# Kernel tuning notes

Measured on AMD Instinct MI355X. Metric: run time of the kernel, lower is better.

## Reference

```python
import jax, jax.numpy as jnp
import numpy as np

DIM, H, HD = 512, 8, 64
N_BANK = 4096
EPS = 1e-5


def layernorm(x, g, b):
    m = jnp.mean(x, axis=-1, keepdims=True)
    v = jnp.mean(jnp.square(x - m), axis=-1, keepdims=True)
    return (x - m) * jax.lax.rsqrt(v + EPS) * g + b


def setup_inputs() -> dict:
    key = jax.random.key(0)
    ks = jax.random.split(key, 8)
    # xavier_uniform bound for square (512,512) linears
    bound = float(np.sqrt(6.0 / (DIM + DIM)))
    inp = {
        "x_q": jax.random.normal(ks[0], (32, 128, DIM), jnp.float32),
        "x_k": jax.random.normal(ks[1], (N_BANK, DIM), jnp.float32),
        "x_v": jax.random.normal(ks[2], (N_BANK, DIM), jnp.float32),
        "Wq": jax.random.uniform(ks[3], (DIM, DIM), jnp.float32, -bound, bound),
        "Wk": jax.random.uniform(ks[4], (DIM, DIM), jnp.float32, -bound, bound),
        "Wv": jax.random.uniform(ks[5], (DIM, DIM), jnp.float32, -bound, bound),
        "Wproj": jax.random.uniform(ks[6], (DIM, DIM), jnp.float32, -bound, bound),
        "qn_g": jnp.ones((HD,), jnp.float32),
        "qn_b": jnp.zeros((HD,), jnp.float32),
        "kn_g": jnp.ones((HD,), jnp.float32),
        "kn_b": jnp.zeros((HD,), jnp.float32),
        "n_g": jnp.ones((DIM,), jnp.float32),
        "n_b": jnp.zeros((DIM,), jnp.float32),
    }
    return inp


def reference(x_q, x_k, x_v, Wq, Wk, Wv, Wproj, qn_g, qn_b, kn_g, kn_b, n_g, n_b):
    B, S, D = x_q.shape
    N = x_k.shape[0]
    scale = HD ** (-0.5)
    # Linear layers (torch: y = x @ W.T)
    q = jnp.einsum('bsd,od->bso', x_q, Wq).reshape(B, S, H, HD).transpose(0, 2, 1, 3)  # (B,H,S,hd)
    k = jnp.einsum('nd,od->no', x_k, Wk).reshape(N, H, HD).transpose(1, 0, 2)          # (H,N,hd)
    v = jnp.einsum('nd,od->no', x_v, Wv).reshape(N, H, HD).transpose(1, 0, 2)          # (H,N,hd)
    # per-head qk layernorm
    q = layernorm(q, qn_g, qn_b) * scale
    k = layernorm(k, kn_g, kn_b)
    # cross-attention to shared bank (K/V have no batch dim)
    attn = jnp.einsum('bhsd,hnd->bhsn', q, k)          # (B,H,S,N)
    attn = jax.nn.softmax(attn, axis=-1)
    x = jnp.einsum('bhsn,hnd->bhsd', attn, v)          # (B,H,S,hd)
    x = x.transpose(0, 2, 1, 3).reshape(B, S, D)
    x = layernorm(x, n_g, n_b)
    x = jnp.einsum('bsd,od->bso', x, Wproj)
    return x
```

## Files before the change

kernel.cpp:

```cpp
#include <hip/hip_runtime.h>
#include <hip/hip_bf16.h>
#include <math.h>

#define DIM 512
#define NHEAD 8
#define HD 64
#define NBANK 4096
#define NQROWS 4096
#define EPS 1e-5f
#define QSCALE 0.125f
#define PART_ELEMS (NQROWS * DIM)

typedef __attribute__((ext_vector_type(4))) float floatx4;
typedef __attribute__((ext_vector_type(8))) short short8;

__device__ __forceinline__ unsigned short f2bf(float f) {
    unsigned int u = __float_as_uint(f);
    u += 0x7fffu + ((u >> 16) & 1u);
    return (unsigned short)(u >> 16);
}
__device__ __forceinline__ float bf2f(unsigned short h) {
    return __uint_as_float(((unsigned int)h) << 16);
}
__device__ __forceinline__ unsigned int pk2(float a, float b) {
    union { __hip_bfloat162 h; unsigned int u; } cvt;
    cvt.h = __float22bfloat162_rn(make_float2(a, b));
    return cvt.u;
}
__device__ __forceinline__ void dma16(const void* gsrc, void* ldst) {
    __builtin_amdgcn_global_load_lds(
        (const __attribute__((address_space(1))) unsigned int*)gsrc,
        (__attribute__((address_space(3))) unsigned int*)ldst, 16, 0, 0);
}

__global__ __launch_bounds__(256) void wcvt_kernel(
    const float* __restrict__ Wq, const float* __restrict__ Wk,
    const float* __restrict__ Wv, const float* __restrict__ Wp,
    unsigned short* __restrict__ Wb)
{
    const float* src = (blockIdx.y == 0) ? Wq : (blockIdx.y == 1) ? Wk
                     : (blockIdx.y == 2) ? Wv : Wp;
    unsigned short* dst = Wb + (size_t)blockIdx.y * DIM * DIM;
    const int i = (blockIdx.x * 256 + threadIdx.x) * 8;
    const int row = i >> 9, kpos = i & 511;
    const int kt = kpos >> 6, seg = (kpos >> 3) & 7;
    const float4 a0 = *(const float4*)(src + i);
    const float4 a1 = *(const float4*)(src + i + 4);
    union { short8 v; unsigned int u[4]; } t;
    t.u[0] = pk2(a0.x, a0.y); t.u[1] = pk2(a0.z, a0.w);
    t.u[2] = pk2(a1.x, a1.y); t.u[3] = pk2(a1.z, a1.w);
    *(short8*)(dst + (size_t)row * 512 + kt * 64 + ((seg ^ (row & 7)) << 3)) = t.v;
}

__global__ __launch_bounds__(256) void qkv_kernel(
    const float* __restrict__ xq, const float* __restrict__ xk, const float* __restrict__ xv,
    const unsigned short* __restrict__ Wb,
    const float* __restrict__ qg, const float* __restrict__ qbeta,
    const float* __restrict__ kg, const float* __restrict__ kbeta,
    unsigned short* __restrict__ Qb, unsigned short* __restrict__ Kb,
    unsigned short* __restrict__ VTb)
{
    __shared__ short8 smem[3072];
    const int tid  = threadIdx.x;
    const int w    = tid >> 6, lane = tid & 63, m = lane & 15, q = lane >> 4;
    const int wr   = w & 1, wc = w >> 1;
    const int row0 = blockIdx.x * 64;
    const int mat  = blockIdx.y >> 2;
    const int col0 = (blockIdx.y & 3) * 128;
    const float* X = (mat == 0) ? xq : (mat == 1) ? xk : xv;
    const unsigned short* Wm = Wb + (size_t)mat * DIM * DIM;

    const int arow0 = tid >> 3,           aseg = tid & 7;
    const int arow1 = (tid + 256) >> 3;
    const float* ap0 = X + (size_t)(row0 + arow0) * DIM + aseg * 8;
    const float* ap1 = X + (size_t)(row0 + arow1) * DIM + aseg * 8;
    const int adst0 = arow0 * 8 + (aseg ^ (arow0 & 7));
    const int adst1 = arow1 * 8 + (aseg ^ (arow1 & 7));
    const unsigned short* bsrc[4];
    #pragma unroll
    for (int j = 0; j < 4; ++j) {
        const int item = j * 256 + tid;
        bsrc[j] = Wm + (size_t)(col0 + (item >> 3)) * DIM + (item & 7) * 8;
    }

    floatx4 acc[2][4];
    #pragma unroll
    for (int mt = 0; mt < 2; ++mt)
        #pragma unroll
        for (int nt = 0; nt < 4; ++nt) acc[mt][nt] = (floatx4){0.f, 0.f, 0.f, 0.f};

    float4 pa[4];
    pa[0] = *(const float4*)(ap0);     pa[1] = *(const float4*)(ap0 + 4);
    pa[2] = *(const float4*)(ap1);     pa[3] = *(const float4*)(ap1 + 4);
    {
        short8* as = smem; short8* bs = smem + 512;
        union { short8 v; unsigned int u[4]; } ta;
        ta.u[0] = pk2(pa[0].x, pa[0].y); ta.u[1] = pk2(pa[0].z, pa[0].w);
        ta.u[2] = pk2(pa[1].x, pa[1].y); ta.u[3] = pk2(pa[1].z, pa[1].w);
        as[adst0] = ta.v;
        ta.u[0] = pk2(pa[2].x, pa[2].y); ta.u[1] = pk2(pa[2].z, pa[2].w);
        ta.u[2] = pk2(pa[3].x, pa[3].y); ta.u[3] = pk2(pa[3].z, pa[3].w);
        as[adst1] = ta.v;
        #pragma unroll
        for (int j = 0; j < 4; ++j)
            dma16(bsrc[j], bs + j * 256 + w * 64);
    }
    pa[0] = *(const float4*)(ap0 + 64);  pa[1] = *(const float4*)(ap0 + 68);
    pa[2] = *(const float4*)(ap1 + 64);  pa[3] = *(const float4*)(ap1 + 68);
    __syncthreads();

    for (int kt = 0; kt < 8; ++kt) {
        short8* as  = smem + (kt & 1) * 1536;
        short8* bs  = as + 512;
        short8* asn = smem + ((kt + 1) & 1) * 1536;
        short8* bsn = asn + 512;
        if (kt < 7) {
            union { short8 v; unsigned int u[4]; } ta;
            ta.u[0] = pk2(pa[0].x, pa[0].y); ta.u[1] = pk2(pa[0].z, pa[0].w);
            ta.u[2] = pk2(pa[1].x, pa[1].y); ta.u[3] = pk2(pa[1].z, pa[1].w);
            asn[adst0] = ta.v;
            ta.u[0] = pk2(pa[2].x, pa[2].y); ta.u[1] = pk2(pa[2].z, pa[2].w);
            ta.u[2] = pk2(pa[3].x, pa[3].y); ta.u[3] = pk2(pa[3].z, pa[3].w);
            asn[adst1] = ta.v;
            #pragma unroll
            for (int j = 0; j < 4; ++j)
                dma16(bsrc[j] + (kt + 1) * 64, bsn + j * 256 + w * 64);
        }
        if (kt < 6) {
            const int o = (kt + 2) * 64;
            pa[0] = *(const float4*)(ap0 + o);  pa[1] = *(const float4*)(ap0 + o + 4);
            pa[2] = *(const float4*)(ap1 + o);  pa[3] = *(const float4*)(ap1 + o + 4);
        }
        #pragma unroll
        for (int s = 0; s < 2; ++s) {
            short8 af[2], bfr[4];
            #pragma unroll
            for (int mt = 0; mt < 2; ++mt)
                af[mt] = as[(wr * 32 + mt * 16 + m) * 8 + ((s * 4 + q) ^ (m & 7))];
            #pragma unroll
            for (int nt = 0; nt < 4; ++nt)
                bfr[nt] = bs[(wc * 64 + nt * 16 + m) * 8 + ((s * 4 + q) ^ (m & 7))];
            #pragma unroll
            for (int mt = 0; mt < 2; ++mt)
                #pragma unroll
                for (int nt = 0; nt < 4; ++nt)
                    acc[mt][nt] = __builtin_amdgcn_mfma_f32_16x16x32_bf16(af[mt], bfr[nt], acc[mt][nt], 0, 0, 0);
        }
        __syncthreads();
    }

    if (mat < 2) {
        const float* g = (mat == 0) ? qg : kg;
        const float* be = (mat == 0) ? qbeta : kbeta;
        unsigned short* Y = (mat == 0) ? Qb : Kb;
        float gv[4], bv[4];
        #pragma unroll
        for (int nt = 0; nt < 4; ++nt) { gv[nt] = g[nt * 16 + m]; bv[nt] = be[nt * 16 + m]; }
        #pragma unroll
        for (int mt = 0; mt < 2; ++mt) {
            #pragma unroll
            for (int r = 0; r < 4; ++r) {
                float s = 0.f, sq = 0.f;
                #pragma unroll
                for (int nt = 0; nt < 4; ++nt) { const float v = acc[mt][nt][r]; s += v; sq += v * v; }
                s  += __shfl_xor(s, 1);  s  += __shfl_xor(s, 2);  s  += __shfl_xor(s, 4);  s  += __shfl_xor(s, 8);
                sq += __shfl_xor(sq, 1); sq += __shfl_xor(sq, 2); sq += __shfl_xor(sq, 4); sq += __shfl_xor(sq, 8);
                const float mean = s * (1.f / HD);
                const float var  = sq * (1.f / HD) - mean * mean;
                const float rr   = rsqrtf(var + EPS);
                const int grow = row0 + wr * 32 + mt * 16 + q * 4 + r;
                #pragma unroll
                for (int nt = 0; nt < 4; ++nt) {
                    float v = (acc[mt][nt][r] - mean) * rr * gv[nt] + bv[nt];
                    if (mat == 0) v *= QSCALE;
                    const int col = col0 + wc * 64 + nt * 16 + m;
                    int scol = col;
                    if (mat == 1) {
                        const int o = col & 63, sg2 = o >> 3;
                        scol = (col & ~63) | (((sg2 ^ (grow & 7)) << 3) | (o & 7));
                    }
                    Y[(size_t)grow * DIM + scol] = f2bf(v);
                }
            }
        }
    } else {
        unsigned short* vt = (unsigned short*)smem;
        __syncthreads();
        #pragma unroll
        for (int mt = 0; mt < 2; ++mt)
            #pragma unroll
            for (int nt = 0; nt < 4; ++nt) {
                const int c  = wc * 64 + nt * 16 + m;
                const int rw = wr * 32 + mt * 16 + q * 4;
                *(unsigned int*)(vt + c * 88 + rw)     = pk2(acc[mt][nt][0], acc[mt][nt][1]);
                *(unsigned int*)(vt + c * 88 + rw + 2) = pk2(acc[mt][nt][2], acc[mt][nt][3]);
            }
        __syncthreads();
        #pragma unroll
        for (int p = 0; p < 4; ++p) {
            const int idx = p * 256 + tid;
            const int c = idx >> 3, g = idx & 7;
            const int dglob = col0 + c, hh = dglob >> 6, dl = dglob & 63;
            const int pos = (g >> 2) * 32 + (g & 3) * 4;
            union { short8 v; ushort4 h4[2]; } tv;
            tv.h4[0] = *(const ushort4*)(vt + c * 88 + pos);
            tv.h4[1] = *(const ushort4*)(vt + c * 88 + pos + 16);
            *(short8*)(VTb + ((size_t)(hh * 64 + blockIdx.x) * 512
                              + dl * 8 + (g ^ (dl & 7))) * 8) = tv.v;
        }
    }
}

__global__ __launch_bounds__(256) void attn_kernel(
    const unsigned short* __restrict__ Qb, const unsigned short* __restrict__ Kb,
    const unsigned short* __restrict__ VTb, unsigned short* __restrict__ AOp,
    float* __restrict__ sums)
{
    __shared__ short8 smem[2048];
    const int tid  = threadIdx.x;
    const int w    = tid >> 6;
    const int lane = tid & 63;
    const int m    = lane & 15;
    const int Qd   = lane >> 4;
    const int h    = blockIdx.x & 7;
    const int qgi  = blockIdx.x >> 3;
    const int row0 = qgi * 128;
    const int part = blockIdx.y;
    const int c0   = part * 16;

    const int it0 = tid, it1 = tid + 256;
    const unsigned short* ksrc0 = Kb + (size_t)(it0 >> 3) * DIM + h * HD + (it0 & 7) * 8;
    const unsigned short* ksrc1 = Kb + (size_t)(it1 >> 3) * DIM + h * HD + (it1 & 7) * 8;
    const unsigned short* vbase = VTb + (size_t)h * 64 * 512 * 8;

    short8 qf[2][2];
    #pragma unroll
    for (int mt = 0; mt < 2; ++mt)
        #pragma unroll
        for (int s = 0; s < 2; ++s)
            qf[mt][s] = *(const short8*)(Qb + (size_t)(row0 + w * 32 + mt * 16 + m) * DIM
                                         + h * HD + s * 32 + Qd * 8);

    floatx4 of[4][2];
    float sump[2] = {0.f, 0.f};
    #pragma unroll
    for (int t = 0; t < 4; ++t)
        #pragma unroll
        for (int mt = 0; mt < 2; ++mt) of[t][mt] = (floatx4){0.f, 0.f, 0.f, 0.f};

    {
        short8* ks = smem; short8* vts = smem + 512;
        dma16(ksrc0 + (size_t)c0 * 64 * DIM, ks + w * 64);
        dma16(ksrc1 + (size_t)c0 * 64 * DIM, ks + 256 + w * 64);
        dma16(vbase + ((size_t)c0 * 512 + it0) * 8, vts + w * 64);
        dma16(vbase + ((size_t)c0 * 512 + it1) * 8, vts + 256 + w * 64);
    }
    __syncthreads();

    for (int c = 0; c < 16; ++c) {
        short8* ks  = smem + (c & 1) * 1024;
        short8* vts = ks + 512;
        if (c < 15) {
            short8* ksn  = smem + ((c + 1) & 1) * 1024;
            short8* vtsn = ksn + 512;
            const size_t nc = c0 + c + 1;
            dma16(ksrc0 + nc * 64 * DIM, ksn + w * 64);
            dma16(ksrc1 + nc * 64 * DIM, ksn + 256 + w * 64);
            dma16(vbase + (nc * 512 + it0) * 8, vtsn + w * 64);
            dma16(vbase + (nc * 512 + it1) * 8, vtsn + 256 + w * 64);
        }

        floatx4 st[4][2];
        #pragma unroll
        for (int t = 0; t < 4; ++t)
            #pragma unroll
            for (int mt = 0; mt < 2; ++mt) st[t][mt] = (floatx4){0.f, 0.f, 0.f, 0.f};
        #pragma unroll
        for (int s = 0; s < 2; ++s)
            #pragma unroll
            for (int t = 0; t < 4; ++t) {
                const short8 kf = ks[(t * 16 + m) * 8 + ((s * 4 + Qd) ^ (m & 7))];
                #pragma unroll
                for (int mt = 0; mt < 2; ++mt)
                    st[t][mt] = __builtin_amdgcn_mfma_f32_16x16x32_bf16(kf, qf[mt][s], st[t][mt], 0, 0, 0);
            }

        float p[4][2][4];
        #pragma unroll
        for (int t = 0; t < 4; ++t)
            #pragma unroll
            for (int mt = 0; mt < 2; ++mt)
                #pragma unroll
                for (int r = 0; r < 4; ++r) {
                    const float e = __expf(st[t][mt][r]);
                    p[t][mt][r] = e;
                    sump[mt] += e;
                }
        union { short8 v; unsigned int u[4]; } pf[2][2];
        #pragma unroll
        for (int mt = 0; mt < 2; ++mt)
            #pragma unroll
            for (int s2 = 0; s2 < 2; ++s2)
                #pragma unroll
                for (int u = 0; u < 4; ++u)
                    pf[mt][s2].u[u] = pk2(p[s2 * 2 + (u >> 1)][mt][(u & 1) * 2],
                                          p[s2 * 2 + (u >> 1)][mt][(u & 1) * 2 + 1]);

        #pragma unroll
        for (int s2 = 0; s2 < 2; ++s2)
            #pragma unroll
            for (int t2 = 0; t2 < 4; ++t2) {
                const short8 vf = vts[(t2 * 16 + m) * 8 + ((s2 * 4 + Qd) ^ (m & 7))];
                #pragma unroll
                for (int mt = 0; mt < 2; ++mt)
                    of[t2][mt] = __builtin_amdgcn_mfma_f32_16x16x32_bf16(vf, pf[mt][s2].v, of[t2][mt], 0, 0, 0);
            }
        __syncthreads();
    }

    #pragma unroll
    for (int mt = 0; mt < 2; ++mt) {
        float s = sump[mt];
        s += __shfl_xor(s, 16);
        s += __shfl_xor(s, 32);
        sump[mt] = s;
    }
    if (Qd == 0) {
        #pragma unroll
        for (int mt = 0; mt < 2; ++mt)
            sums[((size_t)part * NQROWS + row0 + w * 32 + mt * 16 + m) * NHEAD + h] = sump[mt];
    }

    unsigned int* ob = (unsigned int*)smem;
    #pragma unroll
    for (int t2 = 0; t2 < 4; ++t2)
        #pragma unroll
        for (int mt = 0; mt < 2; ++mt) {
            const int qq  = w * 32 + mt * 16 + m;
            const int blk = t2 * 2 + (Qd >> 1);
            const int sub = (Qd & 1) * 2;
            const int bs  = (blk ^ (qq & 7)) * 4;
            ob[qq * 32 + bs + sub]     = pk2(of[t2][mt][0], of[t2][mt][1]);
            ob[qq * 32 + bs + sub + 1] = pk2(of[t2][mt][2], of[t2][mt][3]);
        }
    __syncthreads();
    #pragma unroll
    for (int pp = 0; pp < 4; ++pp) {
        const int idx = tid + pp * 256;
        const int qq = idx >> 3, sg = idx & 7;
        *(short8*)(AOp + (size_t)part * PART_ELEMS + (size_t)(row0 + qq) * DIM + h * HD + sg * 8) =
            smem[qq * 8 + (sg ^ (qq & 7))];
    }
}

__global__ __launch_bounds__(256) void combine_kernel(
    const unsigned short* __restrict__ AOp, const float* __restrict__ sums,
    const float* __restrict__ g, const float* __restrict__ be,
    unsigned short* __restrict__ AO)
{
    __shared__ float rs[256], rq[256], sm[2], sr[2];
    const int tid  = threadIdx.x;
    const int half = tid >> 7;
    const int row  = blockIdx.x * 2 + half;
    const int t    = tid & 127;
    const int h    = t >> 4;

    float stot = 0.f;
    #pragma unroll
    for (int p = 0; p < 4; ++p)
        stot += sums[((size_t)p * NQROWS + row) * NHEAD + h];

    float o[4] = {0.f, 0.f, 0.f, 0.f};
    #pragma unroll
    for (int p = 0; p < 4; ++p) {
        const ushort4 u = *(const ushort4*)(AOp + (size_t)p * PART_ELEMS + (size_t)row * DIM + t * 4);
        o[0] += bf2f(u.x); o[1] += bf2f(u.y); o[2] += bf2f(u.z); o[3] += bf2f(u.w);
    }
    const float inv = 1.0f / stot;
    const float v0 = o[0] * inv, v1 = o[1] * inv, v2 = o[2] * inv, v3 = o[3] * inv;

    rs[tid] = v0 + v1 + v2 + v3;
    rq[tid] = v0 * v0 + v1 * v1 + v2 * v2 + v3 * v3;
    __syncthreads();
    #pragma unroll
    for (int off = 64; off > 0; off >>= 1) {
        if (t < off) { rs[tid] += rs[tid + off]; rq[tid] += rq[tid + off]; }
        __syncthreads();
    }
    if (t == 0) {
        const float mean = rs[tid] * (1.f / DIM);
        const float var  = rq[tid] * (1.f / DIM) - mean * mean;
        sm[half] = mean;
        sr[half] = rsqrtf(var + EPS);
    }
    __syncthreads();

    const float mean = sm[half], rstd = sr[half];
    const float4 g4 = *(const float4*)(g + t * 4);
    const float4 b4 = *(const float4*)(be + t * 4);
    uint2 packed;
    packed.x = pk2((v0 - mean) * rstd * g4.x + b4.x, (v1 - mean) * rstd * g4.y + b4.y);
    packed.y = pk2((v2 - mean) * rstd * g4.z + b4.z, (v3 - mean) * rstd * g4.w + b4.w);
    const int kt = t >> 4, seg = (t >> 1) & 7, jof = (t & 1) * 4;
    *(uint2*)(AO + (size_t)row * DIM + kt * 64 + ((seg ^ (row & 7)) << 3) + jof) = packed;
}

__global__ __launch_bounds__(256) void final_kernel(
    const unsigned short* __restrict__ AO, const unsigned short* __restrict__ Wpb,
    float* __restrict__ out)
{
    __shared__ short8 fs[2048];
    const int tid  = threadIdx.x;
    const int w    = tid >> 6, lane = tid & 63, m = lane & 15, q = lane >> 4;
    const int row0 = blockIdx.x * 64;
    const int col0 = blockIdx.y * 64;

    const int it0 = tid, it1 = tid + 256;
    const unsigned short* asrc0 = AO  + (size_t)(row0 + (it0 >> 3)) * DIM + (it0 & 7) * 8;
    const unsigned short* asrc1 = AO  + (size_t)(row0 + (it1 >> 3)) * DIM + (it1 & 7) * 8;
    const unsigned short* wsrc0 = Wpb + (size_t)(col0 + (it0 >> 3)) * DIM + (it0 & 7) * 8;
    const unsigned short* wsrc1 = Wpb + (size_t)(col0 + (it1 >> 3)) * DIM + (it1 & 7) * 8;

    floatx4 acc[4];
    #pragma unroll
    for (int mt = 0; mt < 4; ++mt) acc[mt] = (floatx4){0.f, 0.f, 0.f, 0.f};

    {
        dma16(asrc0, fs + w * 64);
        dma16(asrc1, fs + 256 + w * 64);
        dma16(wsrc0, fs + 512 + w * 64);
        dma16(wsrc1, fs + 768 + w * 64);
    }
    __syncthreads();

    for (int kt = 0; kt < 8; ++kt) {
        short8* buf  = fs + (kt & 1) * 1024;
        if (kt < 7) {
            short8* bufn = fs + ((kt + 1) & 1) * 1024;
            const int o = (kt + 1) * 64;
            dma16(asrc0 + o, bufn + w * 64);
            dma16(asrc1 + o, bufn + 256 + w * 64);
            dma16(wsrc0 + o, bufn + 512 + w * 64);
            dma16(wsrc1 + o, bufn + 768 + w * 64);
        }
        #pragma unroll
        for (int s = 0; s < 2; ++s) {
            short8 af[4];
            #pragma unroll
            for (int mt = 0; mt < 4; ++mt)
                af[mt] = buf[(mt * 16 + m) * 8 + ((s * 4 + q) ^ (m & 7))];
            const short8 bfr = buf[512 + (w * 16 + m) * 8 + ((s * 4 + q) ^ (m & 7))];
            #pragma unroll
            for (int mt = 0; mt < 4; ++mt)
                acc[mt] = __builtin_amdgcn_mfma_f32_16x16x32_bf16(af[mt], bfr, acc[mt], 0, 0, 0);
        }
        __syncthreads();
    }

    #pragma unroll
    for (int mt = 0; mt < 4; ++mt)
        #pragma unroll
        for (int r = 0; r < 4; ++r)
            out[(size_t)(row0 + mt * 16 + q * 4 + r) * DIM + col0 + w * 16 + m] = acc[mt][r];
}

extern "C" void kernel_launch(void* const* d_in, const int* in_sizes, int n_in,
                              void* d_out, int out_size, void* d_ws, size_t ws_size,
                              hipStream_t stream)
{
    const float* x_q = (const float*)d_in[0];
    const float* x_k = (const float*)d_in[1];
    const float* x_v = (const float*)d_in[2];
    const float* Wq  = (const float*)d_in[3];
    const float* Wk  = (const float*)d_in[4];
    const float* Wv  = (const float*)d_in[5];
    const float* Wp  = (const float*)d_in[6];
    const float* qg  = (const float*)d_in[7];
    const float* qb  = (const float*)d_in[8];
    const float* kg  = (const float*)d_in[9];
    const float* kb  = (const float*)d_in[10];
    const float* ng  = (const float*)d_in[11];
    const float* nb  = (const float*)d_in[12];
    float* out = (float*)d_out;

    unsigned short* Qb   = (unsigned short*)d_ws;
    unsigned short* Kb   = Qb  + (size_t)NQROWS * DIM;
    unsigned short* VTb  = Kb  + (size_t)NBANK * DIM;
    unsigned short* AOp  = VTb + (size_t)NBANK * DIM;
    float*          sums = (float*)(AOp + (size_t)4 * PART_ELEMS);
    unsigned short* Wb   = (unsigned short*)(sums + (size_t)4 * NQROWS * NHEAD);
    unsigned short* AO   = Qb;

    wcvt_kernel<<<dim3(128, 4), 256, 0, stream>>>(Wq, Wk, Wv, Wp, Wb);
    qkv_kernel<<<dim3(64, 12), 256, 0, stream>>>(x_q, x_k, x_v, Wb,
                                                 qg, qb, kg, kb, Qb, Kb, VTb);
    attn_kernel<<<dim3(256, 4), 256, 0, stream>>>(Qb, Kb, VTb, AOp, sums);
    combine_kernel<<<NQROWS / 2, 256, 0, stream>>>(AOp, sums, ng, nb, AO);
    final_kernel<<<dim3(64, 8), 256, 0, stream>>>(AO, Wb + (size_t)3 * DIM * DIM, out);
}
```

Baseline: 169.3 us.

## Pre-convert activations to bf16, DMA A tiles, use exp2 and MFMA row sums

The weight-conversion kernel now also converts x_q, x_k and x_v to swizzled bf16 in a workspace. This lets the QKV GEMM load its A tiles with direct global-to-LDS DMA instead of converting fp32 through registers. In attention, the softmax exponent uses exp2 with log2(e) folded into the Q scale, and row sums are computed with an extra MFMA against a ones vector instead of scalar adds and shuffles. The cost is an extra pass over the inputs plus a bf16 write and re-read, and sums are now taken from bf16-rounded probabilities.

```diff
diff --git a/kernel.cpp b/kernel.cpp
--- a/kernel.cpp
+++ b/kernel.cpp
@@ -8,11 +8,20 @@
 #define NBANK 4096
 #define NQROWS 4096
 #define EPS 1e-5f
-#define QSCALE 0.125f
+#define QSCALE 0.18033688011f
 #define PART_ELEMS (NQROWS * DIM)
 
 typedef __attribute__((ext_vector_type(4))) float floatx4;
 typedef __attribute__((ext_vector_type(8))) short short8;
+
+#if defined(__has_builtin)
+#if __has_builtin(__builtin_amdgcn_exp2f)
+#define EXP2(x) __builtin_amdgcn_exp2f(x)
+#endif
+#endif
+#ifndef EXP2
+#define EXP2(x) __expf((x) * 0.69314718056f)
+#endif
 
 __device__ __forceinline__ unsigned short f2bf(float f) {
     unsigned int u = __float_as_uint(f);
@@ -33,14 +42,24 @@
         (__attribute__((address_space(3))) unsigned int*)ldst, 16, 0, 0);
 }
 
-__global__ __launch_bounds__(256) void wcvt_kernel(
+__global__ __launch_bounds__(256) void cvt_kernel(
     const float* __restrict__ Wq, const float* __restrict__ Wk,
     const float* __restrict__ Wv, const float* __restrict__ Wp,
-    unsigned short* __restrict__ Wb)
-{
-    const float* src = (blockIdx.y == 0) ? Wq : (blockIdx.y == 1) ? Wk
-                     : (blockIdx.y == 2) ? Wv : Wp;
-    unsigned short* dst = Wb + (size_t)blockIdx.y * DIM * DIM;
+    const float* __restrict__ xq, const float* __restrict__ xk,
+    const float* __restrict__ xv,
+    unsigned short* __restrict__ Wb, unsigned short* __restrict__ Xb)
+{
+    const int y = blockIdx.y;
+    const float* src;
+    unsigned short* dst;
+    if (y < 4) {
+        if (blockIdx.x >= 128) return;
+        src = (y == 0) ? Wq : (y == 1) ? Wk : (y == 2) ? Wv : Wp;
+        dst = Wb + (size_t)y * DIM * DIM;
+    } else {
+        src = (y == 4) ? xq : (y == 5) ? xk : xv;
+        dst = Xb + (size_t)(y - 4) * NQROWS * DIM;
+    }
     const int i = (blockIdx.x * 256 + threadIdx.x) * 8;
     const int row = i >> 9, kpos = i & 511;
     const int kt = kpos >> 6, seg = (kpos >> 3) & 7;
@@ -53,8 +72,7 @@
 }
 
 __global__ __launch_bounds__(256) void qkv_kernel(
-    const float* __restrict__ xq, const float* __restrict__ xk, const float* __restrict__ xv,
-    const unsigned short* __restrict__ Wb,
+    const unsigned short* __restrict__ Xb, const unsigned short* __restrict__ Wb,
     const float* __restrict__ qg, const float* __restrict__ qbeta,
     const float* __restrict__ kg, const float* __restrict__ kbeta,
     unsigned short* __restrict__ Qb, unsigned short* __restrict__ Kb,
@@ -67,15 +85,12 @@
     const int row0 = blockIdx.x * 64;
     const int mat  = blockIdx.y >> 2;
     const int col0 = (blockIdx.y & 3) * 128;
-    const float* X = (mat == 0) ? xq : (mat == 1) ? xk : xv;
+    const unsigned short* Xm = Xb + (size_t)mat * NQROWS * DIM;
     const unsigned short* Wm = Wb + (size_t)mat * DIM * DIM;
 
-    const int arow0 = tid >> 3,           aseg = tid & 7;
-    const int arow1 = (tid + 256) >> 3;
-    const float* ap0 = X + (size_t)(row0 + arow0) * DIM + aseg * 8;
-    const float* ap1 = X + (size_t)(row0 + arow1) * DIM + aseg * 8;
-    const int adst0 = arow0 * 8 + (aseg ^ (arow0 & 7));
-    const int adst1 = arow1 * 8 + (aseg ^ (arow1 & 7));
+    const int it0 = tid, it1 = tid + 256;
+    const unsigned short* asrc0 = Xm + (size_t)(row0 + (it0 >> 3)) * DIM + (it0 & 7) * 8;
+    const unsigned short* asrc1 = Xm + (size_t)(row0 + (it1 >> 3)) * DIM + (it1 & 7) * 8;
     const unsigned short* bsrc[4];
     #pragma unroll
     for (int j = 0; j < 4; ++j) {
@@ -89,47 +104,28 @@
         #pragma unroll
         for (int nt = 0; nt < 4; ++nt) acc[mt][nt] = (floatx4){0.f, 0.f, 0.f, 0.f};
 
-    float4 pa[4];
-    pa[0] = *(const float4*)(ap0);     pa[1] = *(const float4*)(ap0 + 4);
-    pa[2] = *(const float4*)(ap1);     pa[3] = *(const float4*)(ap1 + 4);
     {
         short8* as = smem; short8* bs = smem + 512;
-        union { short8 v; unsigned int u[4]; } ta;
-        ta.u[0] = pk2(pa[0].x, pa[0].y); ta.u[1] = pk2(pa[0].z, pa[0].w);
-        ta.u[2] = pk2(pa[1].x, pa[1].y); ta.u[3] = pk2(pa[1].z, pa[1].w);
-        as[adst0] = ta.v;
-        ta.u[0] = pk2(pa[2].x, pa[2].y); ta.u[1] = pk2(pa[2].z, pa[2].w);
-        ta.u[2] = pk2(pa[3].x, pa[3].y); ta.u[3] = pk2(pa[3].z, pa[3].w);
-        as[adst1] = ta.v;
+        dma16(asrc0, as + w * 64);
+        dma16(asrc1, as + 256 + w * 64);
         #pragma unroll
         for (int j = 0; j < 4; ++j)
             dma16(bsrc[j], bs + j * 256 + w * 64);
     }
-    pa[0] = *(const float4*)(ap0 + 64);  pa[1] = *(const float4*)(ap0 + 68);
-    pa[2] = *(const float4*)(ap1 + 64);  pa[3] = *(const float4*)(ap1 + 68);
     __syncthreads();
 
     for (int kt = 0; kt < 8; ++kt) {
-        short8* as  = smem + (kt & 1) * 1536;
-        short8* bs  = as + 512;
-        short8* asn = smem + ((kt + 1) & 1) * 1536;
-        short8* bsn = asn + 512;
+        short8* as = smem + (kt & 1) * 1536;
+        short8* bs = as + 512;
         if (kt < 7) {
-            union { short8 v; unsigned int u[4]; } ta;
-            ta.u[0] = pk2(pa[0].x, pa[0].y); ta.u[1] = pk2(pa[0].z, pa[0].w);
-            ta.u[2] = pk2(pa[1].x, pa[1].y); ta.u[3] = pk2(pa[1].z, pa[1].w);
-            asn[adst0] = ta.v;
-            ta.u[0] = pk2(pa[2].x, pa[2].y); ta.u[1] = pk2(pa[2].z, pa[2].w);
-            ta.u[2] = pk2(pa[3].x, pa[3].y); ta.u[3] = pk2(pa[3].z, pa[3].w);
-            asn[adst1] = ta.v;
+            short8* asn = smem + ((kt + 1) & 1) * 1536;
+            short8* bsn = asn + 512;
+            const int o = (kt + 1) * 64;
+            dma16(asrc0 + o, asn + w * 64);
+            dma16(asrc1 + o, asn + 256 + w * 64);
             #pragma unroll
             for (int j = 0; j < 4; ++j)
-                dma16(bsrc[j] + (kt + 1) * 64, bsn + j * 256 + w * 64);
-        }
-        if (kt < 6) {
-            const int o = (kt + 2) * 64;
-            pa[0] = *(const float4*)(ap0 + o);  pa[1] = *(const float4*)(ap0 + o + 4);
-            pa[2] = *(const float4*)(ap1 + o);  pa[3] = *(const float4*)(ap1 + o + 4);
+                dma16(bsrc[j] + o, bsn + j * 256 + w * 64);
         }
         #pragma unroll
         for (int s = 0; s < 2; ++s) {
@@ -242,11 +238,16 @@
                                          + h * HD + s * 32 + Qd * 8);
 
     floatx4 of[4][2];
-    float sump[2] = {0.f, 0.f};
+    floatx4 sacc[2];
     #pragma unroll
     for (int t = 0; t < 4; ++t)
         #pragma unroll
         for (int mt = 0; mt < 2; ++mt) of[t][mt] = (floatx4){0.f, 0.f, 0.f, 0.f};
+    #pragma unroll
+    for (int mt = 0; mt < 2; ++mt) sacc[mt] = (floatx4){0.f, 0.f, 0.f, 0.f};
+    union { short8 v; unsigned int u[4]; } onesu;
+    #pragma unroll
+    for (int u = 0; u < 4; ++u) onesu.u[u] = 0x3F803F80u;
 
     {
         short8* ks = smem; short8* vts = smem + 512;
@@ -285,26 +286,22 @@
                     st[t][mt] = __builtin_amdgcn_mfma_f32_16x16x32_bf16(kf, qf[mt][s], st[t][mt], 0, 0, 0);
             }
 
-        float p[4][2][4];
-        #pragma unroll
-        for (int t = 0; t < 4; ++t)
-            #pragma unroll
-            for (int mt = 0; mt < 2; ++mt)
-                #pragma unroll
-                for (int r = 0; r < 4; ++r) {
-                    const float e = __expf(st[t][mt][r]);
-                    p[t][mt][r] = e;
-                    sump[mt] += e;
+        union { short8 v; unsigned int u[4]; } pf[2][2];
+        #pragma unroll
+        for (int mt = 0; mt < 2; ++mt)
+            #pragma unroll
+            for (int s2 = 0; s2 < 2; ++s2)
+                #pragma unroll
+                for (int u = 0; u < 4; ++u) {
+                    const int t = s2 * 2 + (u >> 1), r = (u & 1) * 2;
+                    pf[mt][s2].u[u] = pk2(EXP2(st[t][mt][r]), EXP2(st[t][mt][r + 1]));
                 }
-        union { short8 v; unsigned int u[4]; } pf[2][2];
+
         #pragma unroll
         for (int mt = 0; mt < 2; ++mt)
             #pragma unroll
             for (int s2 = 0; s2 < 2; ++s2)
-                #pragma unroll
-                for (int u = 0; u < 4; ++u)
-                    pf[mt][s2].u[u] = pk2(p[s2 * 2 + (u >> 1)][mt][(u & 1) * 2],
-                                          p[s2 * 2 + (u >> 1)][mt][(u & 1) * 2 + 1]);
+                sacc[mt] = __builtin_amdgcn_mfma_f32_16x16x32_bf16(onesu.v, pf[mt][s2].v, sacc[mt], 0, 0, 0);
 
         #pragma unroll
         for (int s2 = 0; s2 < 2; ++s2)
@@ -318,17 +315,10 @@
         __syncthreads();
     }
 
-    #pragma unroll
-    for (int mt = 0; mt < 2; ++mt) {
-        float s = sump[mt];
-        s += __shfl_xor(s, 16);
-        s += __shfl_xor(s, 32);
-        sump[mt] = s;
-    }
     if (Qd == 0) {
         #pragma unroll
         for (int mt = 0; mt < 2; ++mt)
-            sums[((size_t)part * NQROWS + row0 + w * 32 + mt * 16 + m) * NHEAD + h] = sump[mt];
+            sums[((size_t)part * NQROWS + row0 + w * 32 + mt * 16 + m) * NHEAD + h] = sacc[mt][0];
     }
 
     unsigned int* ob = (unsigned int*)smem;
@@ -489,11 +479,11 @@
     unsigned short* AOp  = VTb + (size_t)NBANK * DIM;
     float*          sums = (float*)(AOp + (size_t)4 * PART_ELEMS);
     unsigned short* Wb   = (unsigned short*)(sums + (size_t)4 * NQROWS * NHEAD);
+    unsigned short* Xb   = AOp;
     unsigned short* AO   = Qb;
 
-    wcvt_kernel<<<dim3(128, 4), 256, 0, stream>>>(Wq, Wk, Wv, Wp, Wb);
-    qkv_kernel<<<dim3(64, 12), 256, 0, stream>>>(x_q, x_k, x_v, Wb,
-                                                 qg, qb, kg, kb, Qb, Kb, VTb);
+    cvt_kernel<<<dim3(1024, 7), 256, 0, stream>>>(Wq, Wk, Wv, Wp, x_q, x_k, x_v, Wb, Xb);
+    qkv_kernel<<<dim3(64, 12), 256, 0, stream>>>(Xb, Wb, qg, qb, kg, kb, Qb, Kb, VTb);
     attn_kernel<<<dim3(256, 4), 256, 0, stream>>>(Qb, Kb, VTb, AOp, sums);
     combine_kernel<<<NQROWS / 2, 256, 0, stream>>>(AOp, sums, ng, nb, AO);
     final_kernel<<<dim3(64, 8), 256, 0, stream>>>(AO, Wb + (size_t)3 * DIM * DIM, out);
```

Result: no change. 172.7 us (+2.0%).
